# Optimization experiments

Hardware: AMD Instinct MI355X
Metric: run time of the kernel (lower is better)

## Reference

```python
import jax, jax.numpy as jnp
import numpy as np

N, IN, WS, OUT, H = 50000, 256, 128, 32, 4
E, M, K = 800000, 2, 10
D = OUT * H  # 128
NEG_SLOPE = 0.2


def _decay(n, alpha=1.5):
    k = np.arange(1, n + 1)
    x = 1.0 / np.power(k, alpha)
    return (x / x.sum()).astype(np.float32)


def setup_inputs() -> dict:
    key = jax.random.key(0)
    ks = jax.random.split(key, 16)
    h = jax.random.normal(ks[0], (N, IN), dtype=jnp.float32)
    src0 = jax.random.randint(ks[1], (E,), 0, N, dtype=jnp.int32)
    dst0 = jax.random.randint(ks[2], (E,), 0, N, dtype=jnp.int32)
    src1 = jax.random.randint(ks[3], (E,), 0, N, dtype=jnp.int32)
    dst1 = jax.random.randint(ks[4], (E,), 0, N, dtype=jnp.int32)
    s = 0.05
    Wh = jax.random.normal(ks[5], (WS, IN), dtype=jnp.float32) * s
    # layer 0 (per metapath): fc (H*F, WS), attn_l/attn_r (H, F)
    fc0 = jax.random.normal(ks[6], (M, H * OUT, WS), dtype=jnp.float32) * s
    al0 = jax.random.normal(ks[7], (M, H, OUT), dtype=jnp.float32) * s
    ar0 = jax.random.normal(ks[8], (M, H, OUT), dtype=jnp.float32) * s
    # layer 1 (per metapath): fc (H*F, H*F)
    fc1 = jax.random.normal(ks[9], (M, H * OUT, H * OUT), dtype=jnp.float32) * s
    al1 = jax.random.normal(ks[10], (M, H, OUT), dtype=jnp.float32) * s
    ar1 = jax.random.normal(ks[11], (M, H, OUT), dtype=jnp.float32) * s
    Wp1 = jax.random.normal(ks[12], (128, D), dtype=jnp.float32) * s
    bp1 = jnp.zeros((128,), dtype=jnp.float32)
    Wp2 = jax.random.normal(ks[13], (1, 128), dtype=jnp.float32) * s
    return dict(h=h, src0=src0, dst0=dst0, src1=src1, dst1=dst1, Wh=Wh,
                fc0=fc0, al0=al0, ar0=ar0, fc1=fc1, al1=al1, ar1=ar1,
                Wp1=Wp1, bp1=bp1, Wp2=Wp2)


def gat_layer(x, src, dst, fcW, attn_l, attn_r):
    # x: (N, Din); fcW: (H*F, Din)
    ft = (x @ fcW.T).reshape(N, H, OUT)            # (N, H, F)
    el = jnp.sum(ft * attn_l, axis=-1)             # (N, H)
    er = jnp.sum(ft * attn_r, axis=-1)             # (N, H)
    e = jax.nn.leaky_relu(el[src] + er[dst], NEG_SLOPE)  # (E, H)
    # edge softmax over incoming edges of each destination node
    mx = jax.ops.segment_max(e, dst, num_segments=N)     # (N, H)
    ee = jnp.exp(e - mx[dst])
    sm = jax.ops.segment_sum(ee, dst, num_segments=N)    # (N, H)
    a = ee / sm[dst]                                     # (E, H)
    # global top-k over the edge dimension (th.topk dim=0), per head
    scores, idx = jax.lax.top_k(a.T, K)                  # (H, K)
    scores = jax.nn.softmax(scores, axis=-1)             # softmax over k
    a_new = jnp.zeros_like(a).at[idx, jnp.arange(H)[:, None]].set(scores)
    msg = ft[src] * a_new[:, :, None]                    # (E, H, F)
    out = jax.ops.segment_sum(msg, dst, num_segments=N)  # (N, H, F)
    return jax.nn.elu(out).reshape(N, H * OUT)


def reference(h, src0, dst0, src1, dst1, Wh, fc0, al0, ar0, fc1, al1, ar1, Wp1, bp1, Wp2):
    c = _decay(2, 1.5)
    wh = h @ Wh.T  # (N, WS)
    srcs = (src0, src1)
    dsts = (dst0, dst1)
    embs = []
    for i in range(M):
        a = gat_layer(wh, srcs[i], dsts[i], fc0[i], al0[i], ar0[i])  # (N, D)
        b = gat_layer(a, srcs[i], dsts[i], fc1[i], al1[i], ar1[i])   # (N, D)
        embs.append(a * c[0] + b * c[1])
    z = jnp.stack(embs, axis=1)                                      # (N, M, D)
    w = jnp.tanh(z @ Wp1.T + bp1) @ Wp2.T                            # (N, M, 1)
    beta = jax.nn.softmax(w, axis=1)
    return jnp.sum(beta * z, axis=1)                                 # (N, D)
```

## Files before the change

kernel.cpp:

```cpp
#include <hip/hip_runtime.h>
#include <math.h>

#define NN   50000
#define IN_F 256
#define OUTF 32
#define NH   4
#define NE   800000
#define NM   2
#define NK   10
#define ND   128

#define NCB  782
#define CCAP 1280
#define DSH  6
#define DMSK 63
#define NSL  32
#define SLW  245

__device__ __forceinline__ float lrelu(float x){ return x >= 0.f ? x : 0.2f*x; }
__device__ __forceinline__ unsigned fmap(float f){
  unsigned u = __float_as_uint(f);
  return (u & 0x80000000u) ? ~u : (u | 0x80000000u);
}
__device__ __forceinline__ float funmap(unsigned u){
  return (u & 0x80000000u) ? __uint_as_float(u & 0x7FFFFFFFu) : __uint_as_float(~u);
}

__global__ __launch_bounds__(256) void k_plpr(
    const float* __restrict__ fc0, const float* __restrict__ al0, const float* __restrict__ ar0,
    const float* __restrict__ fc1, const float* __restrict__ al1, const float* __restrict__ ar1,
    float* __restrict__ plpr)
{
  int idx = blockIdx.x*256 + threadIdx.x;
  if (idx >= 4096) return;
  int w  = idx & 127;
  int hh = (idx >> 7) & 3;
  int lr = (idx >> 9) & 1;
  int m  = (idx >> 10) & 1;
  int L  = (idx >> 11) & 1;
  const float* fc = L ? fc1 : fc0;
  const float* at = L ? (lr ? ar1 : al1) : (lr ? ar0 : al0);
  float s = 0.f;
  for (int f = 0; f < OUTF; f++)
    s += at[(m*NH + hh)*OUTF + f] * fc[((size_t)m*128 + hh*OUTF + f)*128 + w];
  plpr[idx] = s;
}

__global__ __launch_bounds__(256) void k_p2(
    const float* __restrict__ plpr, const float* __restrict__ Whm, float* __restrict__ P2)
{
  int idx = blockIdx.x*256 + threadIdx.x;
  if (idx >= 16*256) return;
  int q = idx >> 8, k = idx & 255;
  float s = 0.f;
  for (int w = 0; w < 128; w++)
    s += plpr[q*128 + w] * Whm[(size_t)w*IN_F + k];
  P2[q*256 + k] = s;
}

__global__ __launch_bounds__(256) void k_el(
    const float* __restrict__ hmat, const float* __restrict__ P2,
    float* __restrict__ el0, float* __restrict__ er0)
{
  __shared__ float hs[64][68];
  __shared__ float PL2[16][260];
  int tid = threadIdx.x;
  int r0 = blockIdx.x * 64;
  for (int i = tid; i < 16*64; i += 256){
    int q = i >> 6, k4 = i & 63;
    float4 v = ((const float4*)P2)[q*64 + k4];
    *(float4*)&PL2[q][k4*4] = v;
  }
  int r = tid >> 2, c = tid & 3;
  float a0 = 0.f, a1 = 0.f, a2 = 0.f, a3 = 0.f;
  for (int kc = 0; kc < IN_F; kc += 64){
#pragma unroll
    for (int it = 0; it < 4; it++){
      int item = it*256 + tid;
      int row = item >> 4, f4 = item & 15;
      int grow = r0 + row;
      float4 v = make_float4(0.f,0.f,0.f,0.f);
      if (grow < NN) v = ((const float4*)hmat)[(size_t)grow*64 + (kc >> 2) + f4];
      *(float4*)&hs[row][f4*4] = v;
    }
    __syncthreads();
#pragma unroll
    for (int k4 = 0; k4 < 16; k4++){
      float4 hv = *(const float4*)&hs[r][k4*4];
      float4 u0 = *(const float4*)&PL2[c*4+0][kc + k4*4];
      float4 u1 = *(const float4*)&PL2[c*4+1][kc + k4*4];
      float4 u2 = *(const float4*)&PL2[c*4+2][kc + k4*4];
      float4 u3 = *(const float4*)&PL2[c*4+3][kc + k4*4];
      a0 += hv.x*u0.x; a0 += hv.y*u0.y; a0 += hv.z*u0.z; a0 += hv.w*u0.w;
      a1 += hv.x*u1.x; a1 += hv.y*u1.y; a1 += hv.z*u1.z; a1 += hv.w*u1.w;
      a2 += hv.x*u2.x; a2 += hv.y*u2.y; a2 += hv.z*u2.z; a2 += hv.w*u2.w;
      a3 += hv.x*u3.x; a3 += hv.y*u3.y; a3 += hv.z*u3.z; a3 += hv.w*u3.w;
    }
    __syncthreads();
  }
  int row = r0 + r;
  if (row < NN){
    int m = c >> 1;
    float* dp = (c & 1) ? er0 : el0;
    *(float4*)&dp[((size_t)m*NN + row)*4] = make_float4(a0, a1, a2, a3);
  }
}

__global__ __launch_bounds__(256) void k_part(
    const int* __restrict__ s0, const int* __restrict__ d0,
    const int* __restrict__ s1, const int* __restrict__ d1,
    unsigned* __restrict__ ccnt, unsigned long long* __restrict__ coarse)
{
  int m = blockIdx.y;
  const int* sp = m ? s1 : s0;
  const int* dp = m ? d1 : d0;
  __shared__ unsigned hist[NCB], base[NCB], cur[NCB];
  int tid = threadIdx.x;
  for (int j = tid; j < NCB; j += 256){ hist[j] = 0u; cur[j] = 0u; }
  __syncthreads();
  int per = (NE + gridDim.x - 1) / gridDim.x;
  int e0 = blockIdx.x * per;
  int e1 = e0 + per; if (e1 > NE) e1 = NE;
  for (int i = e0 + tid; i < e1; i += 256)
    atomicAdd(&hist[dp[i] >> DSH], 1u);
  __syncthreads();
  for (int j = tid; j < NCB; j += 256)
    base[j] = hist[j] ? atomicAdd(&ccnt[m*NCB + j], hist[j]) : 0u;
  __syncthreads();
  for (int i = e0 + tid; i < e1; i += 256){
    int d = dp[i];
    int b = d >> DSH;
    unsigned loc = atomicAdd(&cur[b], 1u);
    unsigned pos = base[b] + loc;
    if (pos < CCAP)
      coarse[((size_t)m*NCB + b)*CCAP + pos] =
          ((unsigned long long)(unsigned)i << 24)
        | ((unsigned long long)(unsigned)(d & DMSK) << 16)
        | (unsigned long long)(unsigned)sp[i];
  }
}

__global__ __launch_bounds__(256) void k_fused(
    const unsigned* __restrict__ ccnt, const unsigned long long* __restrict__ coarse,
    const float* __restrict__ el, const float* __restrict__ er,
    unsigned long long* __restrict__ cand)
{
  int bb = blockIdx.x, m = blockIdx.y;
  const unsigned long long* ce = coarse + ((size_t)m*NCB + bb)*CCAP;
  unsigned cnt = ccnt[m*NCB + bb]; if (cnt > CCAP) cnt = CCAP;
  const float* elp = el + (size_t)m*NN*4;
  const float* erp = er + (size_t)m*NN*4;
  int tid = threadIdx.x;
  int h = tid & 3, es = tid >> 2;
  int dbase = bb << DSH;

  __shared__ float4 erL[64];
  __shared__ unsigned mxL[64][4];
  __shared__ unsigned long long smL[64][4];
  __shared__ unsigned metaL[CCAP];
  __shared__ unsigned long long smem_u64[CCAP*2];
  float* eL = (float*)smem_u64;
  unsigned long long (*cs)[NK] = (unsigned long long(*)[NK])smem_u64;

  if (tid < 64){
    int d = dbase + tid;
    erL[tid] = (d < NN) ? *(const float4*)&erp[(size_t)d*4] : make_float4(0.f,0.f,0.f,0.f);
  }
  { int j = tid; mxL[j>>2][j&3] = 0u; smL[j>>2][j&3] = 0ULL; }
  __syncthreads();

  {
    unsigned p = es;
    for (; p + 192 < cnt; p += 256){
      unsigned long long v0 = ce[p], v1 = ce[p+64], v2 = ce[p+128], v3 = ce[p+192];
      float g0 = elp[(unsigned)(v0 & 0xFFFFULL)*4 + h];
      float g1 = elp[(unsigned)(v1 & 0xFFFFULL)*4 + h];
      float g2 = elp[(unsigned)(v2 & 0xFFFFULL)*4 + h];
      float g3 = elp[(unsigned)(v3 & 0xFFFFULL)*4 + h];
      unsigned d0 = (unsigned)((v0 >> 16) & 0xFFULL);
      unsigned d1 = (unsigned)((v1 >> 16) & 0xFFULL);
      unsigned d2 = (unsigned)((v2 >> 16) & 0xFFULL);
      unsigned d3 = (unsigned)((v3 >> 16) & 0xFFULL);
      float e0 = lrelu(g0 + ((const float*)&erL[d0])[h]);
      float e1 = lrelu(g1 + ((const float*)&erL[d1])[h]);
      float e2 = lrelu(g2 + ((const float*)&erL[d2])[h]);
      float e3 = lrelu(g3 + ((const float*)&erL[d3])[h]);
      eL[p*4 + h] = e0; eL[(p+64)*4 + h] = e1;
      eL[(p+128)*4 + h] = e2; eL[(p+192)*4 + h] = e3;
      if (h == 0){
        metaL[p]     = ((unsigned)(v0 >> 24) << 8) | d0;
        metaL[p+64]  = ((unsigned)(v1 >> 24) << 8) | d1;
        metaL[p+128] = ((unsigned)(v2 >> 24) << 8) | d2;
        metaL[p+192] = ((unsigned)(v3 >> 24) << 8) | d3;
      }
      atomicMax(&mxL[d0][h], fmap(e0));
      atomicMax(&mxL[d1][h], fmap(e1));
      atomicMax(&mxL[d2][h], fmap(e2));
      atomicMax(&mxL[d3][h], fmap(e3));
    }
    for (; p < cnt; p += 64){
      unsigned long long v = ce[p];
      unsigned src  = (unsigned)(v & 0xFFFFULL);
      unsigned dloc = (unsigned)((v >> 16) & 0xFFULL);
      float e = lrelu(elp[src*4 + h] + ((const float*)&erL[dloc])[h]);
      eL[p*4 + h] = e;
      if (h == 0) metaL[p] = ((unsigned)(v >> 24) << 8) | dloc;
      atomicMax(&mxL[dloc][h], fmap(e));
    }
  }
  __syncthreads();

  for (unsigned p = es; p < cnt; p += 64){
    unsigned dloc = metaL[p] & 255u;
    float e = eL[p*4 + h];
    atomicAdd(&smL[dloc][h],
        (unsigned long long)llrint((double)expf(e - funmap(mxL[dloc][h])) * 1073741824.0));
  }
  __syncthreads();

  unsigned long long top[NK];
#pragma unroll
  for (int k = 0; k < NK; k++) top[k] = 0ULL;
  for (unsigned p = es; p < cnt; p += 64){
    unsigned mt = metaL[p];
    unsigned dloc = mt & 255u;
    unsigned eid  = mt >> 8;
    float e = eL[p*4 + h];
    float smv = (float)((double)smL[dloc][h] * (1.0/1073741824.0));
    float av = expf(e - funmap(mxL[dloc][h])) / smv;
    unsigned long long key = ((unsigned long long)__float_as_uint(av) << 32)
                           | (unsigned long long)(~eid);
    if (key > top[NK-1]){
#pragma unroll
      for (int k = 0; k < NK; k++){
        unsigned long long hi = key > top[k] ? key : top[k];
        unsigned long long lo = key > top[k] ? top[k] : key;
        top[k] = hi; key = lo;
      }
    }
  }
  __syncthreads();

  int row = h*64 + es;
#pragma unroll
  for (int k = 0; k < NK; k++) cs[row][k] = top[k];
  __syncthreads();
  int w = tid >> 6, lane = tid & 63;
  unsigned long long mytop[NK];
#pragma unroll
  for (int k = 0; k < NK; k++) mytop[k] = cs[w*64 + lane][k];
  unsigned long long best = 0ULL; int bp = -1;
#pragma unroll
  for (int k = 0; k < NK; k++) if (mytop[k] > best){ best = mytop[k]; bp = k; }
  for (int r = 0; r < NK; r++){
    unsigned long long b = best; int srcl = lane;
#pragma unroll
    for (int off = 32; off > 0; off >>= 1){
      unsigned long long ob = __shfl_down(b, off, 64);
      int os = __shfl_down(srcl, off, 64);
      if (ob > b){ b = ob; srcl = os; }
    }
    b = __shfl(b, 0, 64); srcl = __shfl(srcl, 0, 64);
    if (lane == 0) cand[(((size_t)m*NH + w)*NCB + blockIdx.x)*NK + r] = b;
    if (lane == srcl && bp >= 0){
#pragma unroll
      for (int k = 0; k < NK; k++) if (k == bp) mytop[k] = 0ULL;
      best = 0ULL; bp = -1;
#pragma unroll
      for (int k = 0; k < NK; k++) if (mytop[k] > best){ best = mytop[k]; bp = k; }
    }
  }
}

__global__ __launch_bounds__(256) void k_merge1(
    const unsigned long long* __restrict__ cand,
    unsigned long long* __restrict__ cand2)
{
  int hh = blockIdx.x, m = blockIdx.y, z = blockIdx.z;
  int tid = threadIdx.x;
  const unsigned long long* cp = cand + ((size_t)m*NH + hh)*((size_t)NCB*NK);
  int start = z*SLW;
  int end = start + SLW; if (end > NCB*NK) end = NCB*NK;
  unsigned long long mykey = (start + tid < end) ? cp[start + tid] : 0ULL;

  __shared__ unsigned long long red[256];
  __shared__ int redpos[256];
  for (int r = 0; r < NK; r++){
    red[tid] = mykey; redpos[tid] = tid;
    __syncthreads();
    for (int st = 128; st > 0; st >>= 1){
      if (tid < st && red[tid+st] > red[tid]){ red[tid] = red[tid+st]; redpos[tid] = redpos[tid+st]; }
      __syncthreads();
    }
    if (tid == 0)
      cand2[(((size_t)m*NH + hh)*NSL + z)*NK + r] = red[0];
    int winner = redpos[0];
    __syncthreads();
    if (tid == winner) mykey = 0ULL;
  }
}

__global__ __launch_bounds__(256) void k_sel(
    const unsigned long long* __restrict__ cand2,
    const int* __restrict__ s0, const int* __restrict__ d0,
    const int* __restrict__ s1, const int* __restrict__ d1,
    const float* __restrict__ hmat, const float* __restrict__ Whm,
    const float* __restrict__ ftsrc,
    const int* __restrict__ idsA,
    const float* __restrict__ fcW,
    const float* __restrict__ plpr1,
    int* __restrict__ idsOut, float* __restrict__ valsOut,
    float* __restrict__ el2, float* __restrict__ er2, int layer)
{
  int m = blockIdx.x;
  int tid = threadIdx.x;
  const int* sp = m ? s1 : s0;
  const int* dp = m ? d1 : d0;
  int wv = tid >> 6, lane = tid & 63;

  __shared__ unsigned long long selL[NH][NK];
  __shared__ float scL[NH][NK];
  __shared__ int snL[NH][NK], dL[NH][NK];
  __shared__ int slotOf[NH][NK], srcOf[NH][NK];
  __shared__ float whL[NH*NK][132];
  __shared__ float hsrc[NH*NK][260];

  {
    const unsigned long long* cp = cand2 + ((size_t)m*NH + wv)*((size_t)NSL*NK);
    unsigned long long top[NK];
#pragma unroll
    for (int k = 0; k < NK; k++) top[k] = 0ULL;
    for (int i = lane; i < NSL*NK; i += 64){
      unsigned long long key = cp[i];
      if (key > top[NK-1]){
#pragma unroll
        for (int k = 0; k < NK; k++){
          unsigned long long hi = key > top[k] ? key : top[k];
          unsigned long long lo = key > top[k] ? top[k] : key;
          top[k] = hi; key = lo;
        }
      }
    }
    unsigned long long best = 0ULL; int bp = -1;
#pragma unroll
    for (int k = 0; k < NK; k++) if (top[k] > best){ best = top[k]; bp = k; }
    for (int r = 0; r < NK; r++){
      unsigned long long b = best; int srcl = lane;
#pragma unroll
      for (int off = 32; off > 0; off >>= 1){
        unsigned long long ob = __shfl_down(b, off, 64);
        int os = __shfl_down(srcl, off, 64);
        if (ob > b){ b = ob; srcl = os; }
      }
      b = __shfl(b, 0, 64); srcl = __shfl(srcl, 0, 64);
      if (lane == 0) selL[wv][r] = b;
      if (lane == srcl && bp >= 0){
#pragma unroll
        for (int k = 0; k < NK; k++) if (k == bp) top[k] = 0ULL;
        best = 0ULL; bp = -1;
#pragma unroll
        for (int k = 0; k < NK; k++) if (top[k] > best){ best = top[k]; bp = k; }
      }
    }
  }
  __syncthreads();

  if (tid < NH*NK){
    int h = tid / NK, k = tid % NK;
    int e = (int)(~(unsigned)(selL[h][k] & 0xFFFFFFFFULL));
    snL[h][k] = sp[e];
    dL[h][k]  = dp[e];
  }
  __syncthreads();

  if (tid < NH){
    float v0 = __uint_as_float((unsigned)(selL[tid][0] >> 32));
    float p[NK]; float sum = 0.f;
#pragma unroll
    for (int k = 0; k < NK; k++){
      float v = __uint_as_float((unsigned)(selL[tid][k] >> 32));
      p[k] = expf(v - v0); sum += p[k];
    }
#pragma unroll
    for (int k = 0; k < NK; k++) scL[tid][k] = p[k] / sum;
  }

  if (wv == 0){
    int myA = -1;
    if (layer) myA = idsA[m*64 + lane];
    int myid = -1;
    int cnt = 0;
    for (int h = 0; h < NH; h++){
      for (int k = 0; k < NK; k++){
        int sn = snL[h][k], d = dL[h][k];
        int srcslot = sn;
        bool ok = true;
        if (layer){
          unsigned long long mb = __ballot(myA == sn);
          if (mb) srcslot = __ffsll(mb) - 1;
          else ok = false;
        }
        int slot = -1;
        if (ok){
          unsigned long long mm = __ballot(lane < cnt && myid == d);
          if (mm) slot = __ffsll(mm) - 1;
          else { slot = cnt; if (lane == cnt) myid = d; cnt++; }
        }
        if (lane == 0){ slotOf[h][k] = slot; srcOf[h][k] = srcslot; }
      }
    }
    idsOut[m*64 + lane] = (lane < cnt) ? myid : -1;
  }
  __syncthreads();

  if (layer == 0){
    for (int t = tid; t < NH*NK*64; t += 256){
      int e = t >> 6, k4 = t & 63;
      int src = (&snL[0][0])[e];
      float4 v = ((const float4*)hmat)[(size_t)src*64 + k4];
      *(float4*)&hsrc[e][k4*4] = v;
    }
    __syncthreads();
    int w = tid & 127, half = tid >> 7;
    float acc2[20];
#pragma unroll
    for (int i = 0; i < 20; i++) acc2[i] = 0.f;
    const float4* wp = (const float4*)&Whm[(size_t)w*IN_F];
    for (int k4 = 0; k4 < 64; k4++){
      float4 wv2 = wp[k4];
#pragma unroll
      for (int i = 0; i < 20; i++){
        float4 hv = *(const float4*)&hsrc[half + 2*i][k4*4];
        acc2[i] += hv.x*wv2.x; acc2[i] += hv.y*wv2.y;
        acc2[i] += hv.z*wv2.z; acc2[i] += hv.w*wv2.w;
      }
    }
#pragma unroll
    for (int i = 0; i < 20; i++) whL[half + 2*i][w] = acc2[i];
    __syncthreads();
  }

  float* vals = valsOut + (size_t)m*64*128;
  {
    int h = wv, f = lane;
    if (f < OUTF){
      const float* wr = fcW + ((size_t)m*128 + h*OUTF + f)*128;
      for (int k = 0; k < NK; k++){
        int slot = slotOf[h][k];
        if (slot < 0) continue;
        const float* x = layer ? (ftsrc + ((size_t)m*64 + srcOf[h][k])*128)
                               : &whL[h*NK + k][0];
        float dsum = 0.f;
        for (int w = 0; w < 128; w++) dsum += x[w] * wr[w];
        vals[(size_t)slot*128 + h*OUTF + f] += scL[h][k] * dsum;
      }
    }
  }
  __syncthreads();

  for (int t = tid; t < 64*128; t += 256){
    int slot = t >> 7, c = t & 127;
    float x = vals[(size_t)slot*128 + c];
    vals[(size_t)slot*128 + c] = x > 0.f ? x : expm1f(x);
  }
  __syncthreads();

  if (layer == 0){
    for (int t = tid; t < 64*8; t += 256){
      int slot = t >> 3, q = t & 7;
      int d = idsOut[m*64 + slot];
      if (d < 0) continue;
      int lr = q >> 2, hh = q & 3;
      const float* P = plpr1 + (((size_t)m*2 + lr)*NH + hh)*128;
      const float* row = vals + (size_t)slot*128;
      float s = 0.f;
      for (int w = 0; w < 128; w++) s += row[w] * P[w];
      float* dpp = lr ? er2 : el2;
      dpp[((size_t)m*NN + d)*4 + hh] = s;
    }
  }
}

__global__ __launch_bounds__(128) void k_final(
    const int* __restrict__ ids, const float* __restrict__ vals,
    const float* __restrict__ Wp1, const float* __restrict__ bp1, const float* __restrict__ Wp2,
    float c0, float c1, float* __restrict__ out)
{
  int j = blockIdx.x;
  int n = ids[j];
  if (n < 0) return;
  for (int q = 0; q < j; q++) if (ids[q] == n) return;
  int tid = threadIdx.x;
  __shared__ float z[2][128];
  __shared__ int slots[4];
  if (tid < 4){
    int sl = -1;
    const int* base = ids + tid*64;
    for (int q = 0; q < 64; q++) if (base[q] == n){ sl = q; break; }
    slots[tid] = sl;
  }
  __syncthreads();
#pragma unroll
  for (int m = 0; m < 2; m++){
    int sa = slots[m], sb = slots[2 + m];
    float av = sa >= 0 ? vals[((size_t)m*64 + sa)*128 + tid] : 0.f;
    float bv = sb >= 0 ? vals[((size_t)(2 + m)*64 + sb)*128 + tid] : 0.f;
    z[m][tid] = c0*av + c1*bv;
  }
  __syncthreads();
  float a0 = bp1[tid], a1 = a0;
  const float* wr = Wp1 + (size_t)tid*128;
  for (int w = 0; w < 128; w++){
    float wv = wr[w];
    a0 += z[0][w]*wv;
    a1 += z[1][w]*wv;
  }
  float t0 = tanhf(a0), t1 = tanhf(a1);
  float w2v = Wp2[tid];
  __shared__ float r0[128], r1[128];
  r0[tid] = t0*w2v; r1[tid] = t1*w2v;
  __syncthreads();
  for (int st = 64; st > 0; st >>= 1){
    if (tid < st){ r0[tid] += r0[tid+st]; r1[tid] += r1[tid+st]; }
    __syncthreads();
  }
  __shared__ float b0s, b1s;
  if (tid == 0){
    float w0 = r0[0], w1 = r1[0];
    float mxv = fmaxf(w0, w1);
    float e0 = expf(w0 - mxv), e1 = expf(w1 - mxv);
    float s = e0 + e1;
    b0s = e0/s; b1s = e1/s;
  }
  __syncthreads();
  out[(size_t)n*ND + tid] = b0s*z[0][tid] + b1s*z[1][tid];
}

extern "C" void kernel_launch(void* const* d_in, const int* in_sizes, int n_in,
                              void* d_out, int out_size, void* d_ws, size_t ws_size,
                              hipStream_t stream)
{
  const float* h    = (const float*)d_in[0];
  const int*   src0 = (const int*)d_in[1];
  const int*   dst0 = (const int*)d_in[2];
  const int*   src1 = (const int*)d_in[3];
  const int*   dst1 = (const int*)d_in[4];
  const float* Wh   = (const float*)d_in[5];
  const float* fc0  = (const float*)d_in[6];
  const float* al0  = (const float*)d_in[7];
  const float* ar0  = (const float*)d_in[8];
  const float* fc1  = (const float*)d_in[9];
  const float* al1  = (const float*)d_in[10];
  const float* ar1  = (const float*)d_in[11];
  const float* Wp1  = (const float*)d_in[12];
  const float* bp1  = (const float*)d_in[13];
  const float* Wp2  = (const float*)d_in[14];
  float* out = (float*)d_out;

  char* ws = (char*)d_ws;
  size_t off = 0;
  auto alloc = [&](size_t b){ size_t o = off; off = (off + b + 255) & ~(size_t)255; return o; };
  size_t o_el0    = alloc((size_t)NM*NN*4*4);
  size_t o_er0    = alloc((size_t)NM*NN*4*4);
  size_t o_plpr   = alloc(4096*4);
  size_t o_p2     = alloc(16*256*4);
  size_t o_cand   = alloc((size_t)NM*NH*NCB*NK*8);
  size_t o_cand2  = alloc((size_t)NM*NH*NSL*NK*8);
  size_t o_coarse = alloc((size_t)NM*NCB*CCAP*8);
  size_t o_zs     = off;
  size_t o_ccnt   = alloc((size_t)NM*NCB*4);
  size_t o_el2    = alloc((size_t)NM*NN*4*4);
  size_t o_er2    = alloc((size_t)NM*NN*4*4);
  size_t o_vals   = alloc((size_t)2*NM*64*128*4);
  size_t zlen = off - o_zs;
  size_t o_ids    = alloc((size_t)2*NM*64*4);
  (void)ws_size; (void)in_sizes; (void)n_in;

  float* el0p  = (float*)(ws + o_el0);
  float* er0p  = (float*)(ws + o_er0);
  float* plprp = (float*)(ws + o_plpr);
  float* p2p   = (float*)(ws + o_p2);
  unsigned long long* candp  = (unsigned long long*)(ws + o_cand);
  unsigned long long* cand2p = (unsigned long long*)(ws + o_cand2);
  unsigned long long* coarsep = (unsigned long long*)(ws + o_coarse);
  unsigned* ccntp = (unsigned*)(ws + o_ccnt);
  float* el2p  = (float*)(ws + o_el2);
  float* er2p  = (float*)(ws + o_er2);
  float* valsp = (float*)(ws + o_vals);
  int*   idsp  = (int*)(ws + o_ids);
  float* vals0p = valsp;
  float* vals1p = valsp + (size_t)NM*64*128;
  int* ids0p = idsp;
  int* ids1p = idsp + NM*64;
  float* plpr1p = plprp + 2048;

  double x1 = 1.0 / (2.0 * sqrt(2.0));
  double ssum = 1.0 + x1;
  float c0 = (float)(1.0/ssum), c1 = (float)(x1/ssum);

  hipMemsetAsync(d_out, 0, (size_t)out_size*sizeof(float), stream);
  hipMemsetAsync(ws + o_zs, 0, zlen, stream);

  k_plpr<<<16, 256, 0, stream>>>(fc0, al0, ar0, fc1, al1, ar1, plprp);
  k_p2<<<16, 256, 0, stream>>>(plprp, Wh, p2p);
  k_el<<<(NN + 63)/64, 256, 0, stream>>>(h, p2p, el0p, er0p);

  k_part<<<dim3(256, NM), 256, 0, stream>>>(src0, dst0, src1, dst1, ccntp, coarsep);

  dim3 gf(NCB, NM);
  dim3 gm1(NH, NM, NSL);

  k_fused<<<gf, 256, 0, stream>>>(ccntp, coarsep, el0p, er0p, candp);
  k_merge1<<<gm1, 256, 0, stream>>>(candp, cand2p);
  k_sel<<<NM, 256, 0, stream>>>(cand2p, src0, dst0, src1, dst1, h, Wh,
                                (const float*)nullptr, (const int*)nullptr, fc0, plpr1p,
                                ids0p, vals0p, el2p, er2p, 0);

  k_fused<<<gf, 256, 0, stream>>>(ccntp, coarsep, el2p, er2p, candp);
  k_merge1<<<gm1, 256, 0, stream>>>(candp, cand2p);
  k_sel<<<NM, 256, 0, stream>>>(cand2p, src0, dst0, src1, dst1, h, Wh,
                                vals0p, ids0p, fc1, plpr1p,
                                ids1p, vals1p, el2p, er2p, 1);

  k_final<<<256, 128, 0, stream>>>(idsp, valsp, Wp1, bp1, Wp2, c0, c1, out);
}
```

Measured before the change: 341.5 us.

## Split serial top-k selection kernel into parallel merge, select, compute and ELU stages

The single 2-block k_sel kernel is split into four kernels. k_merge2 does the final top-k merge with 512-thread blocks per head and metapath. k_selA resolves edges and slots. k_selB computes the projections per head, across 8 blocks instead of 2. k_elu2 applies ELU and the layer-2 attention projections across 128 blocks. The aim is more parallelism on the tail of each layer, which previously ran on only two workgroups. In exchange it adds several extra kernel launches and global round trips for the intermediate selection data.

After: 302.3 us. 11.5% less time.

```diff
diff --git a/kernel.cpp b/kernel.cpp
--- a/kernel.cpp
+++ b/kernel.cpp
@@ -300,17 +300,38 @@
   }
 }
 
-__global__ __launch_bounds__(256) void k_sel(
+__global__ __launch_bounds__(512) void k_merge2(
     const unsigned long long* __restrict__ cand2,
+    unsigned long long* __restrict__ selg)
+{
+  int hh = blockIdx.x, m = blockIdx.y;
+  int tid = threadIdx.x;
+  const unsigned long long* cp = cand2 + ((size_t)m*NH + hh)*((size_t)NSL*NK);
+  unsigned long long mykey = (tid < NSL*NK) ? cp[tid] : 0ULL;
+
+  __shared__ unsigned long long red[512];
+  __shared__ int redpos[512];
+  for (int r = 0; r < NK; r++){
+    red[tid] = mykey; redpos[tid] = tid;
+    __syncthreads();
+    for (int st = 256; st > 0; st >>= 1){
+      if (tid < st && red[tid+st] > red[tid]){ red[tid] = red[tid+st]; redpos[tid] = redpos[tid+st]; }
+      __syncthreads();
+    }
+    if (tid == 0)
+      selg[((size_t)m*NH + hh)*NK + r] = red[0];
+    int winner = redpos[0];
+    __syncthreads();
+    if (tid == winner) mykey = 0ULL;
+  }
+}
+
+__global__ __launch_bounds__(256) void k_selA(
+    const unsigned long long* __restrict__ selg,
     const int* __restrict__ s0, const int* __restrict__ d0,
     const int* __restrict__ s1, const int* __restrict__ d1,
-    const float* __restrict__ hmat, const float* __restrict__ Whm,
-    const float* __restrict__ ftsrc,
     const int* __restrict__ idsA,
-    const float* __restrict__ fcW,
-    const float* __restrict__ plpr1,
-    int* __restrict__ idsOut, float* __restrict__ valsOut,
-    float* __restrict__ el2, float* __restrict__ er2, int layer)
+    int* __restrict__ idsOut, int4* __restrict__ selinfo, int layer)
 {
   int m = blockIdx.x;
   int tid = threadIdx.x;
@@ -318,67 +339,25 @@
   const int* dp = m ? d1 : d0;
   int wv = tid >> 6, lane = tid & 63;
 
-  __shared__ unsigned long long selL[NH][NK];
   __shared__ float scL[NH][NK];
   __shared__ int snL[NH][NK], dL[NH][NK];
   __shared__ int slotOf[NH][NK], srcOf[NH][NK];
-  __shared__ float whL[NH*NK][132];
-  __shared__ float hsrc[NH*NK][260];
-
-  {
-    const unsigned long long* cp = cand2 + ((size_t)m*NH + wv)*((size_t)NSL*NK);
-    unsigned long long top[NK];
-#pragma unroll
-    for (int k = 0; k < NK; k++) top[k] = 0ULL;
-    for (int i = lane; i < NSL*NK; i += 64){
-      unsigned long long key = cp[i];
-      if (key > top[NK-1]){
-#pragma unroll
-        for (int k = 0; k < NK; k++){
-          unsigned long long hi = key > top[k] ? key : top[k];
-          unsigned long long lo = key > top[k] ? top[k] : key;
-          top[k] = hi; key = lo;
-        }
-      }
-    }
-    unsigned long long best = 0ULL; int bp = -1;
-#pragma unroll
-    for (int k = 0; k < NK; k++) if (top[k] > best){ best = top[k]; bp = k; }
-    for (int r = 0; r < NK; r++){
-      unsigned long long b = best; int srcl = lane;
-#pragma unroll
-      for (int off = 32; off > 0; off >>= 1){
-        unsigned long long ob = __shfl_down(b, off, 64);
-        int os = __shfl_down(srcl, off, 64);
-        if (ob > b){ b = ob; srcl = os; }
-      }
-      b = __shfl(b, 0, 64); srcl = __shfl(srcl, 0, 64);
-      if (lane == 0) selL[wv][r] = b;
-      if (lane == srcl && bp >= 0){
-#pragma unroll
-        for (int k = 0; k < NK; k++) if (k == bp) top[k] = 0ULL;
-        best = 0ULL; bp = -1;
-#pragma unroll
-        for (int k = 0; k < NK; k++) if (top[k] > best){ best = top[k]; bp = k; }
-      }
-    }
-  }
-  __syncthreads();
 
   if (tid < NH*NK){
     int h = tid / NK, k = tid % NK;
-    int e = (int)(~(unsigned)(selL[h][k] & 0xFFFFFFFFULL));
+    unsigned long long s = selg[((size_t)m*NH + h)*NK + k];
+    int e = (int)(~(unsigned)(s & 0xFFFFFFFFULL));
     snL[h][k] = sp[e];
     dL[h][k]  = dp[e];
   }
   __syncthreads();
 
   if (tid < NH){
-    float v0 = __uint_as_float((unsigned)(selL[tid][0] >> 32));
+    float v0 = __uint_as_float((unsigned)(selg[((size_t)m*NH + tid)*NK + 0] >> 32));
     float p[NK]; float sum = 0.f;
 #pragma unroll
     for (int k = 0; k < NK; k++){
-      float v = __uint_as_float((unsigned)(selL[tid][k] >> 32));
+      float v = __uint_as_float((unsigned)(selg[((size_t)m*NH + tid)*NK + k] >> 32));
       p[k] = expf(v - v0); sum += p[k];
     }
 #pragma unroll
@@ -413,71 +392,104 @@
   }
   __syncthreads();
 
+  if (tid < NH*NK){
+    int h = tid / NK, k = tid % NK;
+    selinfo[((size_t)m*NH + h)*NK + k] =
+        make_int4(snL[h][k], slotOf[h][k], srcOf[h][k], __float_as_int(scL[h][k]));
+  }
+}
+
+__global__ __launch_bounds__(256) void k_selB(
+    const int4* __restrict__ selinfo,
+    const float* __restrict__ hmat, const float* __restrict__ Whm,
+    const float* __restrict__ ftsrc,
+    const float* __restrict__ fcW,
+    float* __restrict__ valsOut, int layer)
+{
+  int h = blockIdx.x, m = blockIdx.y;
+  int tid = threadIdx.x;
+  __shared__ int sn10[NK], slot10[NK], srcsl10[NK];
+  __shared__ float sc10[NK];
+  __shared__ float hs10[NK][260];
+  __shared__ float whL10[NK][132];
+  __shared__ float dsumL[NK][32];
+
+  if (tid < NK){
+    int4 si = selinfo[((size_t)m*NH + h)*NK + tid];
+    sn10[tid] = si.x; slot10[tid] = si.y; srcsl10[tid] = si.z;
+    sc10[tid] = __int_as_float(si.w);
+  }
+  __syncthreads();
+
   if (layer == 0){
-    for (int t = tid; t < NH*NK*64; t += 256){
+    for (int t = tid; t < NK*64; t += 256){
       int e = t >> 6, k4 = t & 63;
-      int src = (&snL[0][0])[e];
-      float4 v = ((const float4*)hmat)[(size_t)src*64 + k4];
-      *(float4*)&hsrc[e][k4*4] = v;
-    }
-    __syncthreads();
-    int w = tid & 127, half = tid >> 7;
-    float acc2[20];
-#pragma unroll
-    for (int i = 0; i < 20; i++) acc2[i] = 0.f;
+      float4 v = ((const float4*)hmat)[(size_t)sn10[e]*64 + k4];
+      *(float4*)&hs10[e][k4*4] = v;
+    }
+    __syncthreads();
+    int w = tid & 127, rh = tid >> 7;
+    float acc5[5];
+#pragma unroll
+    for (int i = 0; i < 5; i++) acc5[i] = 0.f;
     const float4* wp = (const float4*)&Whm[(size_t)w*IN_F];
     for (int k4 = 0; k4 < 64; k4++){
       float4 wv2 = wp[k4];
 #pragma unroll
-      for (int i = 0; i < 20; i++){
-        float4 hv = *(const float4*)&hsrc[half + 2*i][k4*4];
-        acc2[i] += hv.x*wv2.x; acc2[i] += hv.y*wv2.y;
-        acc2[i] += hv.z*wv2.z; acc2[i] += hv.w*wv2.w;
+      for (int i = 0; i < 5; i++){
+        float4 hv = *(const float4*)&hs10[rh + 2*i][k4*4];
+        acc5[i] += hv.x*wv2.x; acc5[i] += hv.y*wv2.y;
+        acc5[i] += hv.z*wv2.z; acc5[i] += hv.w*wv2.w;
       }
     }
 #pragma unroll
-    for (int i = 0; i < 20; i++) whL[half + 2*i][w] = acc2[i];
-    __syncthreads();
-  }
-
-  float* vals = valsOut + (size_t)m*64*128;
-  {
-    int h = wv, f = lane;
-    if (f < OUTF){
+    for (int i = 0; i < 5; i++) whL10[rh + 2*i][w] = acc5[i];
+    __syncthreads();
+  }
+
+  for (int t = tid; t < NK*32; t += 256){
+    int k = t >> 5, f = t & 31;
+    float dsum = 0.f;
+    if (slot10[k] >= 0){
+      const float* x = layer ? (ftsrc + ((size_t)m*64 + srcsl10[k])*128) : &whL10[k][0];
       const float* wr = fcW + ((size_t)m*128 + h*OUTF + f)*128;
-      for (int k = 0; k < NK; k++){
-        int slot = slotOf[h][k];
-        if (slot < 0) continue;
-        const float* x = layer ? (ftsrc + ((size_t)m*64 + srcOf[h][k])*128)
-                               : &whL[h*NK + k][0];
-        float dsum = 0.f;
-        for (int w = 0; w < 128; w++) dsum += x[w] * wr[w];
-        vals[(size_t)slot*128 + h*OUTF + f] += scL[h][k] * dsum;
-      }
-    }
-  }
-  __syncthreads();
-
-  for (int t = tid; t < 64*128; t += 256){
-    int slot = t >> 7, c = t & 127;
-    float x = vals[(size_t)slot*128 + c];
-    vals[(size_t)slot*128 + c] = x > 0.f ? x : expm1f(x);
-  }
-  __syncthreads();
-
-  if (layer == 0){
-    for (int t = tid; t < 64*8; t += 256){
-      int slot = t >> 3, q = t & 7;
-      int d = idsOut[m*64 + slot];
-      if (d < 0) continue;
-      int lr = q >> 2, hh = q & 3;
-      const float* P = plpr1 + (((size_t)m*2 + lr)*NH + hh)*128;
-      const float* row = vals + (size_t)slot*128;
-      float s = 0.f;
-      for (int w = 0; w < 128; w++) s += row[w] * P[w];
-      float* dpp = lr ? er2 : el2;
-      dpp[((size_t)m*NN + d)*4 + hh] = s;
-    }
+      for (int w = 0; w < 128; w++) dsum += x[w] * wr[w];
+    }
+    dsumL[k][f] = dsum;
+  }
+  __syncthreads();
+
+  if (tid < OUTF){
+    int f = tid;
+    float* vals = valsOut + (size_t)m*64*128;
+    for (int k = 0; k < NK; k++){
+      int slot = slot10[k];
+      if (slot < 0) continue;
+      vals[(size_t)slot*128 + h*OUTF + f] += sc10[k] * dsumL[k][f];
+    }
+  }
+}
+
+__global__ __launch_bounds__(128) void k_elu2(
+    const int* __restrict__ ids, float* __restrict__ vals,
+    const float* __restrict__ plpr1,
+    float* __restrict__ el2, float* __restrict__ er2, int doEl2)
+{
+  int slot = blockIdx.x, m = blockIdx.y, tid = threadIdx.x;
+  float* row = vals + ((size_t)m*64 + slot)*128;
+  float x = row[tid];
+  row[tid] = x > 0.f ? x : expm1f(x);
+  __syncthreads();
+  if (!doEl2) return;
+  int d = ids[m*64 + slot];
+  if (d < 0) return;
+  if (tid < 8){
+    int lr = tid >> 2, hh = tid & 3;
+    const float* P = plpr1 + (((size_t)m*2 + lr)*NH + hh)*128;
+    float s = 0.f;
+    for (int w = 0; w < 128; w++) s += row[w] * P[w];
+    float* dp = lr ? er2 : el2;
+    dp[((size_t)m*NN + d)*4 + hh] = s;
   }
 }
 
@@ -566,6 +578,8 @@
   size_t o_p2     = alloc(16*256*4);
   size_t o_cand   = alloc((size_t)NM*NH*NCB*NK*8);
   size_t o_cand2  = alloc((size_t)NM*NH*NSL*NK*8);
+  size_t o_selg   = alloc((size_t)NM*NH*NK*8);
+  size_t o_selinf = alloc((size_t)NM*NH*NK*16);
   size_t o_coarse = alloc((size_t)NM*NCB*CCAP*8);
   size_t o_zs     = off;
   size_t o_ccnt   = alloc((size_t)NM*NCB*4);
@@ -582,6 +596,8 @@
   float* p2p   = (float*)(ws + o_p2);
   unsigned long long* candp  = (unsigned long long*)(ws + o_cand);
   unsigned long long* cand2p = (unsigned long long*)(ws + o_cand2);
+  unsigned long long* selgp  = (unsigned long long*)(ws + o_selg);
+  int4* selinfp = (int4*)(ws + o_selinf);
   unsigned long long* coarsep = (unsigned long long*)(ws + o_coarse);
   unsigned* ccntp = (unsigned*)(ws + o_ccnt);
   float* el2p  = (float*)(ws + o_el2);
@@ -609,18 +625,25 @@
 
   dim3 gf(NCB, NM);
   dim3 gm1(NH, NM, NSL);
+  dim3 gm2(NH, NM);
+  dim3 gb(NH, NM);
+  dim3 ge(64, NM);
 
   k_fused<<<gf, 256, 0, stream>>>(ccntp, coarsep, el0p, er0p, candp);
   k_merge1<<<gm1, 256, 0, stream>>>(candp, cand2p);
-  k_sel<<<NM, 256, 0, stream>>>(cand2p, src0, dst0, src1, dst1, h, Wh,
-                                (const float*)nullptr, (const int*)nullptr, fc0, plpr1p,
-                                ids0p, vals0p, el2p, er2p, 0);
+  k_merge2<<<gm2, 512, 0, stream>>>(cand2p, selgp);
+  k_selA<<<NM, 256, 0, stream>>>(selgp, src0, dst0, src1, dst1,
+                                 (const int*)nullptr, ids0p, selinfp, 0);
+  k_selB<<<gb, 256, 0, stream>>>(selinfp, h, Wh, (const float*)nullptr, fc0, vals0p, 0);
+  k_elu2<<<ge, 128, 0, stream>>>(ids0p, vals0p, plpr1p, el2p, er2p, 1);
 
   k_fused<<<gf, 256, 0, stream>>>(ccntp, coarsep, el2p, er2p, candp);
   k_merge1<<<gm1, 256, 0, stream>>>(candp, cand2p);
-  k_sel<<<NM, 256, 0, stream>>>(cand2p, src0, dst0, src1, dst1, h, Wh,
-                                vals0p, ids0p, fc1, plpr1p,
-                                ids1p, vals1p, el2p, er2p, 1);
+  k_merge2<<<gm2, 512, 0, stream>>>(cand2p, selgp);
+  k_selA<<<NM, 256, 0, stream>>>(selgp, src0, dst0, src1, dst1,
+                                 ids0p, ids1p, selinfp, 1);
+  k_selB<<<gb, 256, 0, stream>>>(selinfp, h, Wh, vals0p, fc1, vals1p, 1);
+  k_elu2<<<ge, 128, 0, stream>>>(ids1p, vals1p, plpr1p, el2p, er2p, 0);
 
   k_final<<<256, 128, 0, stream>>>(idsp, valsp, Wp1, bp1, Wp2, c0, c1, out);
 }
```
